# Kernel tuning notes

Measured on AMD Instinct MI355X. Metric: run time of the kernel, lower is better.

The kernel has to match this reference:

```python
import jax, jax.numpy as jnp
import numpy as np

T, B, A, OBS = 128, 16, 32, 256
K, NACT, HID = 3, 9, 32


def setup_inputs() -> dict:
    key = jax.random.key(0)
    ks = jax.random.split(key, 12)
    sc = 0.1  # small init scale for stability
    d = {}
    d["x"] = jax.random.normal(ks[0], (T, B, A, OBS), jnp.float32)
    d["done"] = jax.random.randint(ks[1], (T, B), 0, 2, jnp.int32)
    d["actions"] = jax.random.randint(ks[2], (T, B, A, K), 0, NACT, jnp.int32)
    d["W1"] = sc * jax.random.normal(ks[3], (128, OBS), jnp.float32)
    d["b1"] = jnp.zeros((128,), jnp.float32)
    d["W2"] = sc * jax.random.normal(ks[4], (128, 128), jnp.float32)
    d["b2"] = jnp.zeros((128,), jnp.float32)
    d["W3"] = sc * jax.random.normal(ks[5], (64, 128), jnp.float32)
    d["b3"] = jnp.zeros((64,), jnp.float32)
    d["Wih"] = sc * jax.random.normal(ks[6], (4 * HID, 64), jnp.float32)
    d["Whh"] = sc * jax.random.normal(ks[7], (4 * HID, HID), jnp.float32)
    d["bih"] = jnp.zeros((4 * HID,), jnp.float32)
    d["bhh"] = jnp.zeros((4 * HID,), jnp.float32)
    d["Wh"] = sc * jax.random.normal(ks[8], (K, NACT, HID), jnp.float32)
    d["bh"] = jnp.zeros((K, NACT), jnp.float32)
    d["h0"] = jnp.zeros((B * A, HID), jnp.float32)
    d["c0"] = jnp.zeros((B * A, HID), jnp.float32)
    return d


def _forward(x, done, actions, W1, b1, W2, b2, W3, b3,
             Wih, Whh, bih, bhh, Wh, bh, h0, c0):
    # MLP trunk: n_obs -> 128 -> 128 -> 64 (tanh, tanh, linear)
    z = jnp.tanh(x @ W1.T + b1)
    z = jnp.tanh(z @ W2.T + b2)
    z = z @ W3.T + b3                       # [T, B, A, 64]
    zf = z.reshape(T, B * A, 64)
    # done[t] repeated per agent (repeat_interleave along batch*agent axis)
    done_f = jnp.repeat(done.astype(x.dtype), A, axis=1)  # [T, B*A]

    def step(carry, inp):
        h, c = carry
        zt, dt = inp                        # [B*A,64], [B*A]
        mask = (1.0 - dt)[:, None]
        h = h * mask
        c = c * mask
        gates = zt @ Wih.T + bih + h @ Whh.T + bhh  # [B*A, 4H]
        i, f, g, o = jnp.split(gates, 4, axis=-1)   # PyTorch gate order i,f,g,o
        i, f, o = jax.nn.sigmoid(i), jax.nn.sigmoid(f), jax.nn.sigmoid(o)
        g = jnp.tanh(g)
        c = f * c + i * g
        h = o * jnp.tanh(c)
        return (h, c), h

    (_, _), ys = jax.lax.scan(step, (h0, c0), (zf, done_f))
    y = ys.reshape(T, B, A, HID)
    # multi-head categorical logits: stacked heads [K, NACT, HID]
    logits = jnp.einsum('tbah,knh->tbakn', y, Wh) + bh  # [T,B,A,K,NACT]
    lp = jax.nn.log_softmax(logits, axis=-1)
    entropies = -jnp.sum(jnp.exp(lp) * lp, axis=-1)     # [T,B,A,K]
    alp = jnp.take_along_axis(lp, actions[..., None], axis=-1)[..., 0]  # [T,B,A,K]
    logprobs = jnp.prod(alp, axis=-1)  # faithful: product of per-head log-probs
    return logprobs, entropies


def reference(x, done, actions, W1, b1, W2, b2, W3, b3,
              Wih, Whh, bih, bhh, Wh, bh, h0, c0):
    logprobs, entropies = _forward(x, done, actions, W1, b1, W2, b2, W3, b3,
                                   Wih, Whh, bih, bhh, Wh, bh, h0, c0)
    return actions, logprobs, entropies
```

## Files before the change

### kernel.cpp

```cpp
#include <hip/hip_runtime.h>
#include <math.h>

namespace {
constexpr int Tn = 128, Bn = 16, An = 32, OBS = 256, Kh = 3, NACT = 9, HID = 32;
constexpr int TBA = Tn * Bn * An;
constexpr int BA  = Bn * An;
constexpr int OUT_LP  = TBA * Kh;
constexpr int OUT_ENT = TBA * Kh + TBA;

constexpr int W1_OFF  = 0;
constexpr int W2_OFF  = 32768;
constexpr int W3_OFF  = 49152;
constexpr int WIH_OFF = 57344;
constexpr int W16_TOT = 65536;

typedef __fp16   pk16x2 __attribute__((ext_vector_type(2)));
typedef _Float16 half4v __attribute__((ext_vector_type(4)));
typedef _Float16 half8v __attribute__((ext_vector_type(8)));
typedef float    f32x4  __attribute__((ext_vector_type(4)));
}

__device__ __forceinline__ float fast_sig(float x) {
  return __builtin_amdgcn_rcpf(1.f + __expf(-x));
}
__device__ __forceinline__ float fast_tanh(float x) {
  return fmaf(2.f, fast_sig(2.f * x), -1.f);
}
__device__ __forceinline__ unsigned h2bits(pk16x2 h) {
  return __builtin_bit_cast(unsigned, h);
}
__device__ __forceinline__ pk16x2 bits2h(unsigned u) {
  return __builtin_bit_cast(pk16x2, u);
}

__device__ __forceinline__ float dot2(pk16x2 a, pk16x2 b, float c) {
#if __has_builtin(__builtin_amdgcn_fdot2)
  return __builtin_amdgcn_fdot2(a, b, c, false);
#else
  c = fmaf((float)a.x, (float)b.x, c);
  return fmaf((float)a.y, (float)b.y, c);
#endif
}

__global__ __launch_bounds__(256) void cvtw_kernel(
    const float* __restrict__ W1, const float* __restrict__ W2,
    const float* __restrict__ W3, const float* __restrict__ Wih,
    _Float16* __restrict__ w16)
{
  int i = blockIdx.x * 256 + threadIdx.x;
  float v;
  if (i < W2_OFF)       v = W1[i];
  else if (i < W3_OFF)  v = W2[i - W2_OFF];
  else if (i < WIH_OFF) v = W3[i - W3_OFF];
  else                  v = Wih[i - WIH_OFF];
  w16[i] = (_Float16)v;
}

template<int ROWS, int WSTR>
__device__ __forceinline__ void stage_wh(const _Float16* __restrict__ Wg, int kofs,
                                         _Float16* __restrict__ wt, int tid)
{
#pragma unroll
  for (int it = 0; it < ROWS/32; ++it) {
    int idx = tid + it*256;
    int o = idx >> 3, g8 = idx & 7;
    *(half8v*)&wt[o*72 + g8*8] =
        *(const half8v*)&Wg[(size_t)o*WSTR + kofs + g8*8];
  }
}

template<int NOC, int XSTR>
__device__ __forceinline__ void mfma_slab(const _Float16* __restrict__ xsrc,
                                          const _Float16* __restrict__ wt,
                                          int rA, int ln, int quad, f32x4 acc[8])
{
#pragma unroll
  for (int kc = 0; kc < 2; ++kc) {
    half8v a = *(const half8v*)&xsrc[rA*XSTR + kc*32 + quad*8];
#pragma unroll
    for (int oc = 0; oc < NOC; ++oc) {
      half8v b = *(const half8v*)&wt[(oc*16 + ln)*72 + kc*32 + quad*8];
      acc[oc] = __builtin_amdgcn_mfma_f32_16x16x32_f16(a, b, acc[oc], 0, 0, 0);
    }
  }
}

__global__ __launch_bounds__(256) void mlp_kernel(
    const float* __restrict__ x, const _Float16* __restrict__ w16,
    const float* __restrict__ b1, const float* __restrict__ b2,
    const float* __restrict__ b3, const float* __restrict__ bih,
    const float* __restrict__ bhh, unsigned* __restrict__ G1p)
{
  __shared__ __align__(16) _Float16 xs[64*72];
  __shared__ __align__(16) _Float16 wt[128*72];
  __shared__ __align__(16) _Float16 act[64*136];
  const _Float16* W1h  = w16 + W1_OFF;
  const _Float16* W2h  = w16 + W2_OFF;
  const _Float16* W3h  = w16 + W3_OFF;
  const _Float16* Wihh = w16 + WIH_OFF;
  const int tid  = threadIdx.x;
  const int w    = tid >> 6;
  const int lane = tid & 63;
  const int ln   = lane & 15;
  const int quad = lane >> 4;
  const int rA   = 16*w + ln;
  const int r0   = 16*w + quad*4;
  const int R0   = blockIdx.x * 64;
  f32x4 acc[8];

#pragma unroll
  for (int oc = 0; oc < 8; ++oc) acc[oc] = (f32x4)0.f;
  for (int kt = 0; kt < 4; ++kt) {
#pragma unroll
    for (int it = 0; it < 2; ++it) {
      int idx = tid + it*256;
      int r = idx >> 3, g8 = idx & 7;
      const float* xp = &x[(size_t)(R0 + r)*OBS + kt*64 + g8*8];
      float4 v0 = *(const float4*)xp;
      float4 v1 = *(const float4*)(xp + 4);
      half8v hv = { (_Float16)v0.x, (_Float16)v0.y, (_Float16)v0.z, (_Float16)v0.w,
                    (_Float16)v1.x, (_Float16)v1.y, (_Float16)v1.z, (_Float16)v1.w };
      *(half8v*)&xs[r*72 + g8*8] = hv;
    }
    stage_wh<128, 256>(W1h, kt*64, wt, tid);
    __syncthreads();
    mfma_slab<8, 72>(xs, wt, rA, ln, quad, acc);
    __syncthreads();
  }
#pragma unroll
  for (int oc = 0; oc < 8; ++oc) {
    int o = oc*16 + ln;
    float bv = b1[o];
#pragma unroll
    for (int r = 0; r < 4; ++r)
      act[(r0 + r)*136 + o] = (_Float16)fast_tanh(acc[oc][r] + bv);
  }

#pragma unroll
  for (int oc = 0; oc < 8; ++oc) acc[oc] = (f32x4)0.f;
  for (int kt = 0; kt < 2; ++kt) {
    stage_wh<128, 128>(W2h, kt*64, wt, tid);
    __syncthreads();
    mfma_slab<8, 136>(act + kt*64, wt, rA, ln, quad, acc);
    __syncthreads();
  }
#pragma unroll
  for (int oc = 0; oc < 8; ++oc) {
    int o = oc*16 + ln;
    float bv = b2[o];
#pragma unroll
    for (int r = 0; r < 4; ++r)
      act[(r0 + r)*136 + o] = (_Float16)fast_tanh(acc[oc][r] + bv);
  }

#pragma unroll
  for (int oc = 0; oc < 4; ++oc) acc[oc] = (f32x4)0.f;
  for (int kt = 0; kt < 2; ++kt) {
    stage_wh<64, 128>(W3h, kt*64, wt, tid);
    __syncthreads();
    mfma_slab<4, 136>(act + kt*64, wt, rA, ln, quad, acc);
    __syncthreads();
  }
#pragma unroll
  for (int oc = 0; oc < 4; ++oc) {
    int o = oc*16 + ln;
    float bv = b3[o];
#pragma unroll
    for (int r = 0; r < 4; ++r)
      xs[(r0 + r)*72 + o] = (_Float16)(acc[oc][r] + bv);
  }

#pragma unroll
  for (int oc = 0; oc < 8; ++oc) acc[oc] = (f32x4)0.f;
  stage_wh<128, 64>(Wihh, 0, wt, tid);
  __syncthreads();
  mfma_slab<8, 72>(xs, wt, rA, ln, quad, acc);
#pragma unroll
  for (int oc = 0; oc < 4; ++oc) {
    int o  = oc*16 + ln;
    int oh = o + 64;
    float blo = bih[o]  + bhh[o];
    float bhi = bih[oh] + bhh[oh];
#pragma unroll
    for (int r = 0; r < 4; ++r) {
      pk16x2 p = __builtin_amdgcn_cvt_pkrtz(acc[oc][r] + blo, acc[oc+4][r] + bhi);
      G1p[(size_t)(R0 + r0 + r)*64 + o] = h2bits(p);
    }
  }
}

__global__ __launch_bounds__(64) void lstm_kernel(
    const unsigned* __restrict__ G1p, const float* __restrict__ Whh,
    const int* __restrict__ done, const float* __restrict__ h0,
    const float* __restrict__ c0, unsigned* __restrict__ Y16)
{
  __shared__ float md[Tn];
  const int lane = threadIdx.x;
  const int u = lane & 31;
  const int row = blockIdx.x;
  const int b = row >> 5;

  pk16x2 wlo[16], whi[16];
#pragma unroll
  for (int k4 = 0; k4 < 8; ++k4) {
    float4 a = *(const float4*)&Whh[lane*HID + k4*4];
    float4 bq = *(const float4*)&Whh[(64 + lane)*HID + k4*4];
    wlo[2*k4+0] = __builtin_amdgcn_cvt_pkrtz(a.x, a.y);
    wlo[2*k4+1] = __builtin_amdgcn_cvt_pkrtz(a.z, a.w);
    whi[2*k4+0] = __builtin_amdgcn_cvt_pkrtz(bq.x, bq.y);
    whi[2*k4+1] = __builtin_amdgcn_cvt_pkrtz(bq.z, bq.w);
  }
  md[lane]      = 1.f - (float)done[lane*Bn + b];
  md[lane + 64] = 1.f - (float)done[(lane + 64)*Bn + b];
  float c = c0[row*HID + u];
  float h = h0[row*HID + u];
  __syncthreads();

  float hsw = __shfl_xor(h, 1);
  unsigned pk = h2bits(__builtin_amdgcn_cvt_pkrtz(h, hsw));

  const float sA = (lane < 32) ? 2.f : 1.f;
  const float cA = (lane < 32) ? 2.f : 1.f;
  const float cB = (lane < 32) ? -1.f : 0.f;

  const size_t rb = (size_t)row*64;
  unsigned gA = G1p[rb + lane];
  unsigned gB = G1p[(size_t)BA*64 + rb + lane];
  unsigned gC = G1p[(size_t)2*BA*64 + rb + lane];
  float mA = md[0], mB = md[1], mC = md[2];

  for (int t = 0; t < Tn; ++t) {
    unsigned gp = gA; gA = gB; gB = gC;
    float m = mA; mA = mB; mB = mC;
    int tp = t + 3; tp = (tp < Tn) ? tp : (Tn - 1);
    gC = G1p[(size_t)tp*BA*64 + rb + lane];
    mC = md[tp];

    unsigned hp[16];
#pragma unroll
    for (int k = 0; k < 16; ++k)
      hp[k] = __builtin_amdgcn_readlane(pk, 2*k);

    pk16x2 gph = bits2h(gp);
    float pl[4] = { 0.f, 0.f, 0.f, 0.f };
    float ph[4] = { 0.f, 0.f, 0.f, 0.f };
#pragma unroll
    for (int k = 0; k < 16; ++k) {
      int p = k & 3;
      pk16x2 hk = bits2h(hp[k]);
      pl[p] = dot2(wlo[k], hk, pl[p]);
      ph[p] = dot2(whi[k], hk, ph[p]);
    }
    float gl = fmaf(m, (pl[0] + pl[1]) + (pl[2] + pl[3]), (float)gph.x);
    float gh = fmaf(m, (ph[0] + ph[1]) + (ph[2] + ph[3]), (float)gph.y);

    float slo = fast_sig(gl);
    float ahi = fmaf(cA, fast_sig(sA * gh), cB);
    unsigned pr = h2bits(__builtin_amdgcn_cvt_pkrtz(slo, ahi));
    unsigned qr = __shfl_xor(pr, 32);
    pk16x2 qh = bits2h(qr);
    float fv = (float)qh.x;
    float ov = (float)qh.y;

    c = fmaf(fv, m * c, slo * ahi);
    h = ov * fast_tanh(c);

    hsw = __shfl_xor(h, 1);
    pk = h2bits(__builtin_amdgcn_cvt_pkrtz(h, hsw));
    if ((lane & 33) == 0)
      Y16[((size_t)t*BA + row)*16 + (u >> 1)] = pk;
  }
}

__global__ __launch_bounds__(256) void head_kernel(
    const unsigned* __restrict__ Y16, const float* __restrict__ Wh,
    const float* __restrict__ bh, const int* __restrict__ actions,
    float* __restrict__ out)
{
  __shared__ __align__(16) float whs[27*32];
  __shared__ float bhs[32];
  const int tid = threadIdx.x;
  const int R0 = blockIdx.x * 256;
  for (int i = tid; i < 27*32; i += 256) whs[i] = Wh[i];
  if (tid < 27) bhs[tid] = bh[tid];
  const int row = R0 + tid;
  float yv[32];
#pragma unroll
  for (int i4 = 0; i4 < 4; ++i4) {
    uint4 yw = *(const uint4*)&Y16[(size_t)row*16 + i4*4];
    pk16x2 p0 = bits2h(yw.x), p1 = bits2h(yw.y), p2 = bits2h(yw.z), p3 = bits2h(yw.w);
    yv[i4*8+0] = (float)p0.x; yv[i4*8+1] = (float)p0.y;
    yv[i4*8+2] = (float)p1.x; yv[i4*8+3] = (float)p1.y;
    yv[i4*8+4] = (float)p2.x; yv[i4*8+5] = (float)p2.y;
    yv[i4*8+6] = (float)p3.x; yv[i4*8+7] = (float)p3.y;
  }
  __syncthreads();
  float l[27];
#pragma unroll
  for (int m = 0; m < 27; ++m) {
    float a = bhs[m];
#pragma unroll
    for (int k4 = 0; k4 < 8; ++k4) {
      float4 w4 = *(const float4*)&whs[m*32 + k4*4];
      a = fmaf(yv[k4*4+0], w4.x, a);
      a = fmaf(yv[k4*4+1], w4.y, a);
      a = fmaf(yv[k4*4+2], w4.z, a);
      a = fmaf(yv[k4*4+3], w4.w, a);
    }
    l[m] = a;
  }
  float logprob = 1.0f;
#pragma unroll
  for (int kk = 0; kk < 3; ++kk) {
    float mx = l[kk*9];
#pragma unroll
    for (int n = 1; n < 9; ++n) mx = fmaxf(mx, l[kk*9+n]);
    float s = 0.f;
#pragma unroll
    for (int n = 0; n < 9; ++n) s += __expf(l[kk*9+n] - mx);
    float lse = mx + __logf(s);
    float ent = 0.f;
#pragma unroll
    for (int n = 0; n < 9; ++n) {
      float lp = l[kk*9+n] - lse;
      ent -= __expf(lp) * lp;
    }
    int a = actions[row*3 + kk];
    float alp = 0.f;
#pragma unroll
    for (int n = 0; n < 9; ++n) alp = (a == n) ? (l[kk*9+n] - lse) : alp;
    logprob *= alp;
    out[row*3 + kk] = (float)a;
    out[OUT_ENT + row*3 + kk] = ent;
  }
  out[OUT_LP + row] = logprob;
}

extern "C" void kernel_launch(void* const* d_in, const int* in_sizes, int n_in,
                              void* d_out, int out_size, void* d_ws, size_t ws_size,
                              hipStream_t stream)
{
  const float* x       = (const float*)d_in[0];
  const int*   done    = (const int*)  d_in[1];
  const int*   actions = (const int*)  d_in[2];
  const float* W1  = (const float*)d_in[3];
  const float* b1  = (const float*)d_in[4];
  const float* W2  = (const float*)d_in[5];
  const float* b2  = (const float*)d_in[6];
  const float* W3  = (const float*)d_in[7];
  const float* b3  = (const float*)d_in[8];
  const float* Wih = (const float*)d_in[9];
  const float* Whh = (const float*)d_in[10];
  const float* bih = (const float*)d_in[11];
  const float* bhh = (const float*)d_in[12];
  const float* Wh  = (const float*)d_in[13];
  const float* bh  = (const float*)d_in[14];
  const float* h0  = (const float*)d_in[15];
  const float* c0  = (const float*)d_in[16];
  float* out = (float*)d_out;

  unsigned* G1p = (unsigned*)d_ws;
  unsigned* Y16 = G1p + (size_t)TBA*64;
  _Float16* W16 = (_Float16*)(Y16 + (size_t)TBA*16);

  cvtw_kernel<<<W16_TOT/256, 256, 0, stream>>>(W1, W2, W3, Wih, W16);
  mlp_kernel<<<TBA/64, 256, 0, stream>>>(x, W16, b1, b2, b3, bih, bhh, G1p);
  lstm_kernel<<<BA, 64, 0, stream>>>(G1p, Whh, done, h0, c0, Y16);
  head_kernel<<<TBA/256, 256, 0, stream>>>(Y16, Wh, bh, actions, out);
}
```

Measured before the change: 204.2 us.

## Compute all four LSTM gates per lane, dropping the cross-half gate shuffle

The LSTM recurrence now keeps all four gate weight rows for one hidden unit in each lane. Before, the 64 lanes each held two gates and swapped results with a shuffle across the two wave halves. The MLP kernel writes the precomputed input gates as one uint2 per unit, packing (i,g) and (f,o), and the recurrence loop is unrolled by four with a prefetch distance of four. This removes one shuffle and the packing step from the serial critical path. In exchange each lane does twice the dot-product work, the upper 32 lanes do duplicate work, and register pressure rises.

```diff
diff --git a/kernel.cpp b/kernel.cpp
--- a/kernel.cpp
+++ b/kernel.cpp
@@ -15,7 +15,6 @@
 constexpr int W16_TOT = 65536;
 
 typedef __fp16   pk16x2 __attribute__((ext_vector_type(2)));
-typedef _Float16 half4v __attribute__((ext_vector_type(4)));
 typedef _Float16 half8v __attribute__((ext_vector_type(8)));
 typedef float    f32x4  __attribute__((ext_vector_type(4)));
 }
@@ -32,7 +31,6 @@
 __device__ __forceinline__ pk16x2 bits2h(unsigned u) {
   return __builtin_bit_cast(pk16x2, u);
 }
-
 __device__ __forceinline__ float dot2(pk16x2 a, pk16x2 b, float c) {
 #if __has_builtin(__builtin_amdgcn_fdot2)
   return __builtin_amdgcn_fdot2(a, b, c, false);
@@ -89,7 +87,7 @@
     const float* __restrict__ x, const _Float16* __restrict__ w16,
     const float* __restrict__ b1, const float* __restrict__ b2,
     const float* __restrict__ b3, const float* __restrict__ bih,
-    const float* __restrict__ bhh, unsigned* __restrict__ G1p)
+    const float* __restrict__ bhh, uint2* __restrict__ G1q)
 {
   __shared__ __align__(16) _Float16 xs[64*72];
   __shared__ __align__(16) _Float16 wt[128*72];
@@ -176,21 +174,25 @@
   __syncthreads();
   mfma_slab<8, 72>(xs, wt, rA, ln, quad, acc);
 #pragma unroll
-  for (int oc = 0; oc < 4; ++oc) {
-    int o  = oc*16 + ln;
-    int oh = o + 64;
-    float blo = bih[o]  + bhh[o];
-    float bhi = bih[oh] + bhh[oh];
+  for (int p = 0; p < 2; ++p) {
+    int ui = p*16 + ln;
+    float bi = bih[ui]      + bhh[ui];
+    float bf = bih[ui + 32] + bhh[ui + 32];
+    float bg = bih[ui + 64] + bhh[ui + 64];
+    float bo = bih[ui + 96] + bhh[ui + 96];
 #pragma unroll
     for (int r = 0; r < 4; ++r) {
-      pk16x2 p = __builtin_amdgcn_cvt_pkrtz(acc[oc][r] + blo, acc[oc+4][r] + bhi);
-      G1p[(size_t)(R0 + r0 + r)*64 + o] = h2bits(p);
+      int n = R0 + r0 + r;
+      uint2 q;
+      q.x = h2bits(__builtin_amdgcn_cvt_pkrtz(acc[p  ][r] + bi, acc[p+4][r] + bg));
+      q.y = h2bits(__builtin_amdgcn_cvt_pkrtz(acc[p+2][r] + bf, acc[p+6][r] + bo));
+      G1q[(size_t)n*32 + ui] = q;
     }
   }
 }
 
 __global__ __launch_bounds__(64) void lstm_kernel(
-    const unsigned* __restrict__ G1p, const float* __restrict__ Whh,
+    const uint2* __restrict__ G1q, const float* __restrict__ Whh,
     const int* __restrict__ done, const float* __restrict__ h0,
     const float* __restrict__ c0, unsigned* __restrict__ Y16)
 {
@@ -200,15 +202,21 @@
   const int row = blockIdx.x;
   const int b = row >> 5;
 
-  pk16x2 wlo[16], whi[16];
+  pk16x2 wi[16], wf[16], wg[16], wo[16];
 #pragma unroll
   for (int k4 = 0; k4 < 8; ++k4) {
-    float4 a = *(const float4*)&Whh[lane*HID + k4*4];
-    float4 bq = *(const float4*)&Whh[(64 + lane)*HID + k4*4];
-    wlo[2*k4+0] = __builtin_amdgcn_cvt_pkrtz(a.x, a.y);
-    wlo[2*k4+1] = __builtin_amdgcn_cvt_pkrtz(a.z, a.w);
-    whi[2*k4+0] = __builtin_amdgcn_cvt_pkrtz(bq.x, bq.y);
-    whi[2*k4+1] = __builtin_amdgcn_cvt_pkrtz(bq.z, bq.w);
+    float4 a  = *(const float4*)&Whh[(u      )*HID + k4*4];
+    float4 bq = *(const float4*)&Whh[(u + 32 )*HID + k4*4];
+    float4 cq = *(const float4*)&Whh[(u + 64 )*HID + k4*4];
+    float4 dq = *(const float4*)&Whh[(u + 96 )*HID + k4*4];
+    wi[2*k4+0] = __builtin_amdgcn_cvt_pkrtz(a.x,  a.y);
+    wi[2*k4+1] = __builtin_amdgcn_cvt_pkrtz(a.z,  a.w);
+    wf[2*k4+0] = __builtin_amdgcn_cvt_pkrtz(bq.x, bq.y);
+    wf[2*k4+1] = __builtin_amdgcn_cvt_pkrtz(bq.z, bq.w);
+    wg[2*k4+0] = __builtin_amdgcn_cvt_pkrtz(cq.x, cq.y);
+    wg[2*k4+1] = __builtin_amdgcn_cvt_pkrtz(cq.z, cq.w);
+    wo[2*k4+0] = __builtin_amdgcn_cvt_pkrtz(dq.x, dq.y);
+    wo[2*k4+1] = __builtin_amdgcn_cvt_pkrtz(dq.z, dq.w);
   }
   md[lane]      = 1.f - (float)done[lane*Bn + b];
   md[lane + 64] = 1.f - (float)done[(lane + 64)*Bn + b];
@@ -219,57 +227,53 @@
   float hsw = __shfl_xor(h, 1);
   unsigned pk = h2bits(__builtin_amdgcn_cvt_pkrtz(h, hsw));
 
-  const float sA = (lane < 32) ? 2.f : 1.f;
-  const float cA = (lane < 32) ? 2.f : 1.f;
-  const float cB = (lane < 32) ? -1.f : 0.f;
-
-  const size_t rb = (size_t)row*64;
-  unsigned gA = G1p[rb + lane];
-  unsigned gB = G1p[(size_t)BA*64 + rb + lane];
-  unsigned gC = G1p[(size_t)2*BA*64 + rb + lane];
-  float mA = md[0], mB = md[1], mC = md[2];
-
-  for (int t = 0; t < Tn; ++t) {
-    unsigned gp = gA; gA = gB; gB = gC;
-    float m = mA; mA = mB; mB = mC;
-    int tp = t + 3; tp = (tp < Tn) ? tp : (Tn - 1);
-    gC = G1p[(size_t)tp*BA*64 + rb + lane];
-    mC = md[tp];
-
-    unsigned hp[16];
-#pragma unroll
-    for (int k = 0; k < 16; ++k)
-      hp[k] = __builtin_amdgcn_readlane(pk, 2*k);
-
-    pk16x2 gph = bits2h(gp);
-    float pl[4] = { 0.f, 0.f, 0.f, 0.f };
-    float ph[4] = { 0.f, 0.f, 0.f, 0.f };
-#pragma unroll
-    for (int k = 0; k < 16; ++k) {
-      int p = k & 3;
-      pk16x2 hk = bits2h(hp[k]);
-      pl[p] = dot2(wlo[k], hk, pl[p]);
-      ph[p] = dot2(whi[k], hk, ph[p]);
-    }
-    float gl = fmaf(m, (pl[0] + pl[1]) + (pl[2] + pl[3]), (float)gph.x);
-    float gh = fmaf(m, (ph[0] + ph[1]) + (ph[2] + ph[3]), (float)gph.y);
-
-    float slo = fast_sig(gl);
-    float ahi = fmaf(cA, fast_sig(sA * gh), cB);
-    unsigned pr = h2bits(__builtin_amdgcn_cvt_pkrtz(slo, ahi));
-    unsigned qr = __shfl_xor(pr, 32);
-    pk16x2 qh = bits2h(qr);
-    float fv = (float)qh.x;
-    float ov = (float)qh.y;
-
-    c = fmaf(fv, m * c, slo * ahi);
-    h = ov * fast_tanh(c);
-
-    hsw = __shfl_xor(h, 1);
-    pk = h2bits(__builtin_amdgcn_cvt_pkrtz(h, hsw));
-    if ((lane & 33) == 0)
-      Y16[((size_t)t*BA + row)*16 + (u >> 1)] = pk;
-  }
+  const uint2* gbase = G1q + (size_t)row*32 + u;
+  const size_t gstride = (size_t)BA*32;
+  uint2 q0 = gbase[0*gstride];
+  uint2 q1 = gbase[1*gstride];
+  uint2 q2 = gbase[2*gstride];
+  uint2 q3 = gbase[3*gstride];
+
+#define LSTM_PHASE(TT, Q)                                                \
+  {                                                                      \
+    uint2 cur = Q;                                                       \
+    int tnx = (TT) + 4; tnx = (tnx < Tn) ? tnx : (Tn - 1);               \
+    Q = gbase[(size_t)tnx * gstride];                                    \
+    float m = md[(TT)];                                                  \
+    unsigned hp[16];                                                     \
+    _Pragma("unroll") for (int k = 0; k < 16; ++k)                       \
+      hp[k] = __builtin_amdgcn_readlane(pk, 2*k);                        \
+    float ai0=0.f, ai1=0.f, af0=0.f, af1=0.f;                            \
+    float ag0=0.f, ag1=0.f, ao0=0.f, ao1=0.f;                            \
+    _Pragma("unroll") for (int k = 0; k < 16; k += 2) {                  \
+      pk16x2 ha = bits2h(hp[k]), hb = bits2h(hp[k+1]);                   \
+      ai0 = dot2(wi[k], ha, ai0); ai1 = dot2(wi[k+1], hb, ai1);          \
+      af0 = dot2(wf[k], ha, af0); af1 = dot2(wf[k+1], hb, af1);          \
+      ag0 = dot2(wg[k], ha, ag0); ag1 = dot2(wg[k+1], hb, ag1);          \
+      ao0 = dot2(wo[k], ha, ao0); ao1 = dot2(wo[k+1], hb, ao1);          \
+    }                                                                    \
+    pk16x2 ig = bits2h(cur.x), fo = bits2h(cur.y);                       \
+    float gi = fmaf(m, ai0 + ai1, (float)ig.x);                          \
+    float gf = fmaf(m, af0 + af1, (float)fo.x);                          \
+    float gg = fmaf(m, ag0 + ag1, (float)ig.y);                          \
+    float go = fmaf(m, ao0 + ao1, (float)fo.y);                          \
+    float iv = fast_sig(gi), fv = fast_sig(gf);                          \
+    float gv = fast_tanh(gg), ov = fast_sig(go);                         \
+    c = fmaf(fv, m * c, iv * gv);                                        \
+    h = ov * fast_tanh(c);                                               \
+    float hx = __shfl_xor(h, 1);                                         \
+    pk = h2bits(__builtin_amdgcn_cvt_pkrtz(h, hx));                      \
+    if ((lane & 33) == 0)                                                \
+      Y16[((size_t)(TT)*BA + row)*16 + (u >> 1)] = pk;                   \
+  }
+
+  for (int t = 0; t < Tn; t += 4) {
+    LSTM_PHASE(t + 0, q0)
+    LSTM_PHASE(t + 1, q1)
+    LSTM_PHASE(t + 2, q2)
+    LSTM_PHASE(t + 3, q3)
+  }
+#undef LSTM_PHASE
 }
 
 __global__ __launch_bounds__(256) void head_kernel(
@@ -359,12 +363,12 @@
   const float* c0  = (const float*)d_in[16];
   float* out = (float*)d_out;
 
-  unsigned* G1p = (unsigned*)d_ws;
-  unsigned* Y16 = G1p + (size_t)TBA*64;
+  uint2* G1q = (uint2*)d_ws;
+  unsigned* Y16 = (unsigned*)(G1q + (size_t)TBA*32);
   _Float16* W16 = (_Float16*)(Y16 + (size_t)TBA*16);
 
   cvtw_kernel<<<W16_TOT/256, 256, 0, stream>>>(W1, W2, W3, Wih, W16);
-  mlp_kernel<<<TBA/64, 256, 0, stream>>>(x, W16, b1, b2, b3, bih, bhh, G1p);
-  lstm_kernel<<<BA, 64, 0, stream>>>(G1p, Whh, done, h0, c0, Y16);
+  mlp_kernel<<<TBA/64, 256, 0, stream>>>(x, W16, b1, b2, b3, bih, bhh, G1q);
+  lstm_kernel<<<BA, 64, 0, stream>>>(G1q, Whh, done, h0, c0, Y16);
   head_kernel<<<TBA/256, 256, 0, stream>>>(Y16, Wh, bh, actions, out);
 }
```

Measured after the change: 200.7 us. Within noise of the previous version (-1.7%).
